# Kernel optimization log

Hardware: AMD Instinct MI355X
Metric: run time of the kernel (lower is better)

## Reference

```python
import jax, jax.numpy as jnp
import numpy as np

C = 512
GROUPS = 32
EPS = 1e-6


def setup_inputs() -> dict:
    key = jax.random.key(0)
    ks = jax.random.split(key, 10)
    B, H, W = 4, 64, 64
    s = 1.0 / np.sqrt(C)
    return {
        "x": jax.random.normal(ks[0], (B, C, H, W), dtype=jnp.float32),
        "gn_weight": jnp.ones((C,), jnp.float32),
        "gn_bias": jnp.zeros((C,), jnp.float32),
        "Wq": jax.random.normal(ks[1], (C, C), jnp.float32) * s,
        "bq": jnp.zeros((C,), jnp.float32),
        "Wk": jax.random.normal(ks[2], (C, C), jnp.float32) * s,
        "bk": jnp.zeros((C,), jnp.float32),
        "Wv": jax.random.normal(ks[3], (C, C), jnp.float32) * s,
        "bv": jnp.zeros((C,), jnp.float32),
        "Wo": jax.random.normal(ks[4], (C, C), jnp.float32) * s,
        "bo": jnp.zeros((C,), jnp.float32),
    }


def _group_norm(x, weight, bias):
    B, Ch, H, W = x.shape
    xg = x.reshape(B, GROUPS, Ch // GROUPS, H, W)
    mean = jnp.mean(xg, axis=(2, 3, 4), keepdims=True)
    var = jnp.var(xg, axis=(2, 3, 4), keepdims=True)
    xg = (xg - mean) * jax.lax.rsqrt(var + EPS)
    h = xg.reshape(B, Ch, H, W)
    return h * weight[None, :, None, None] + bias[None, :, None, None]


def reference(x, gn_weight, gn_bias, Wq, bq, Wk, bk, Wv, bv, Wo, bo):
    B, Ch, H, W = x.shape
    h = _group_norm(x, gn_weight, gn_bias)
    # [B, N, C] with N = H*W spatial tokens
    h = h.reshape(B, Ch, H * W).transpose(0, 2, 1)
    q = h @ Wq.T + bq
    k = h @ Wk.T + bk
    v = h @ Wv.T + bv
    scale = 1.0 / jnp.sqrt(jnp.asarray(Ch, x.dtype))
    scores = jnp.einsum("bnc,bmc->bnm", q, k) * scale  # [B, N, N]
    attn = jax.nn.softmax(scores, axis=-1)
    out = jnp.einsum("bnm,bmc->bnc", attn, v)
    out = out @ Wo.T + bo  # Dropout(0.0) is identity
    out = out.transpose(0, 2, 1).reshape(B, Ch, H, W)
    return x + out
```

## Files before the change

kernel.cpp:

```cpp
#include <hip/hip_runtime.h>
#include <hip/hip_bf16.h>

typedef __attribute__((ext_vector_type(8))) short bf16x8;
typedef __attribute__((ext_vector_type(4))) short bf16x4;
typedef __attribute__((ext_vector_type(4))) float f32x4;

__device__ __forceinline__ short f2bf(float f){
  __hip_bfloat16 h = __float2bfloat16(f);
  return __builtin_bit_cast(short, h);
}
__device__ __forceinline__ float bf2f(short s){
  unsigned u = ((unsigned)(unsigned short)s) << 16;
  return __builtin_bit_cast(float, u);
}

__device__ __forceinline__ void gload_lds16(const short* g, char* l){
  __builtin_amdgcn_global_load_lds(
      (const __attribute__((address_space(1))) void*)g,
      (__attribute__((address_space(3))) void*)l, 16, 0, 0);
}

#define SB0() __builtin_amdgcn_sched_barrier(0)
#define LGKM0() do{ asm volatile("s_waitcnt lgkmcnt(0)" ::: "memory"); SB0(); }while(0)
#define LGKM4() do{ asm volatile("s_waitcnt lgkmcnt(4)" ::: "memory"); SB0(); }while(0)

__global__ __launch_bounds__(256) void gn_stats(const float* __restrict__ x,
                                                float* __restrict__ stats){
  int b = blockIdx.x >> 5, g = blockIdx.x & 31;
  const float4* p = (const float4*)(x + ((long long)b*512 + g*16)*4096);
  float s = 0.f, s2 = 0.f;
  for (int i = threadIdx.x; i < 16384; i += 256){
    float4 v = p[i];
    s  += v.x + v.y + v.z + v.w;
    s2 += v.x*v.x + v.y*v.y + v.z*v.z + v.w*v.w;
  }
  #pragma unroll
  for (int o = 32; o; o >>= 1){ s += __shfl_xor(s, o); s2 += __shfl_xor(s2, o); }
  __shared__ float rs[4], rs2[4];
  int wid = threadIdx.x >> 6;
  if ((threadIdx.x & 63) == 0){ rs[wid] = s; rs2[wid] = s2; }
  __syncthreads();
  if (threadIdx.x == 0){
    float S  = rs[0]+rs[1]+rs[2]+rs[3];
    float S2 = rs2[0]+rs2[1]+rs2[2]+rs2[3];
    float mean = S * (1.f/65536.f);
    float var  = S2 * (1.f/65536.f) - mean*mean;
    stats[blockIdx.x*2]   = mean;
    stats[blockIdx.x*2+1] = rsqrtf(var + 1e-6f);
  }
}

__global__ __launch_bounds__(256) void gn_apply(const float* __restrict__ x,
                                                const float* __restrict__ stats,
                                                const float* __restrict__ gw,
                                                const float* __restrict__ gb,
                                                short* __restrict__ h){
  __shared__ float tile[128][65];
  int b  = blockIdx.y;
  int n0 = blockIdx.x * 64;
  int t  = threadIdx.x;
  const float* xb = x + (long long)b*512*4096;
  for (int cc = 0; cc < 4; cc++){
    int c0 = cc*128;
    #pragma unroll
    for (int r = 0; r < 128; r += 4){
      int c = r + (t >> 6);
      tile[c][t & 63] = xb[(long long)(c0+c)*4096 + n0 + (t & 63)];
    }
    __syncthreads();
    int n = t >> 2, cp = (t & 3)*32;
    short tmp[32];
    #pragma unroll
    for (int j = 0; j < 32; j++){
      int c = c0 + cp + j;
      float mean = stats[(b*32 + (c >> 4))*2];
      float rstd = stats[(b*32 + (c >> 4))*2 + 1];
      float v = (tile[cp+j][n] - mean)*rstd*gw[c] + gb[c];
      tmp[j] = f2bf(v);
    }
    long long ho = ((long long)b*4096 + n0 + n)*512 + c0 + cp;
    #pragma unroll
    for (int j2 = 0; j2 < 4; j2++){
      bf16x8 v8;
      #pragma unroll
      for (int e = 0; e < 8; e++) v8[e] = tmp[j2*8 + e];
      *(bf16x8*)&h[ho + j2*8] = v8;
    }
    __syncthreads();
  }
}

__global__ __launch_bounds__(256) void f2bf_all(
    const float* __restrict__ w0, const float* __restrict__ w1,
    const float* __restrict__ w2, const float* __restrict__ w3,
    short* __restrict__ o0, short* __restrict__ o1,
    short* __restrict__ o2, short* __restrict__ o3){
  int idx = blockIdx.x*256 + threadIdx.x;
  int m = idx >> 15, r = idx & 32767;
  const float* src = (m==0) ? w0 : (m==1) ? w1 : (m==2) ? w2 : w3;
  short* dst       = (m==0) ? o0 : (m==1) ? o1 : (m==2) ? o2 : o3;
  const float4* p = (const float4*)src + (long long)r*2;
  float4 a = p[0], c = p[1];
  bf16x8 v;
  v[0]=f2bf(a.x); v[1]=f2bf(a.y); v[2]=f2bf(a.z); v[3]=f2bf(a.w);
  v[4]=f2bf(c.x); v[5]=f2bf(c.y); v[6]=f2bf(c.z); v[7]=f2bf(c.w);
  *(bf16x8*)&dst[(long long)r*8] = v;
}

__global__ __launch_bounds__(256) void softmax_rows(short* __restrict__ S){
  long long row = blockIdx.x;
  short* p = S + row*4096;
  int t = threadIdx.x;
  bf16x8 v0 = *(bf16x8*)&p[t*16];
  bf16x8 v1 = *(bf16x8*)&p[t*16 + 8];
  float f[16];
  #pragma unroll
  for (int e = 0; e < 8; e++){ f[e] = bf2f(v0[e]); f[8+e] = bf2f(v1[e]); }
  float m = f[0];
  #pragma unroll
  for (int e = 1; e < 16; e++) m = fmaxf(m, f[e]);
  #pragma unroll
  for (int o = 32; o; o >>= 1) m = fmaxf(m, __shfl_xor(m, o));
  __shared__ float red[4];
  int wid = t >> 6;
  if ((t & 63) == 0) red[wid] = m;
  __syncthreads();
  m = fmaxf(fmaxf(red[0], red[1]), fmaxf(red[2], red[3]));
  float s = 0.f;
  #pragma unroll
  for (int e = 0; e < 16; e++){ f[e] = exp2f((f[e]-m)*1.4426950408889634f); s += f[e]; }
  #pragma unroll
  for (int o = 32; o; o >>= 1) s += __shfl_xor(s, o);
  __syncthreads();
  if ((t & 63) == 0) red[wid] = s;
  __syncthreads();
  s = red[0]+red[1]+red[2]+red[3];
  float inv = 1.f/s;
  #pragma unroll
  for (int e = 0; e < 8; e++){ v0[e] = f2bf(f[e]*inv); v1[e] = f2bf(f[8+e]*inv); }
  *(bf16x8*)&p[t*16]     = v0;
  *(bf16x8*)&p[t*16 + 8] = v1;
}

template<int MODE, int BN, bool SWZ>
__global__ __launch_bounds__(512, 2) void gemmP(
    const short* __restrict__ A, const short* __restrict__ Bw,
    const float* __restrict__ bias,
    void* __restrict__ outp, const float* __restrict__ resid,
    int M, int Nn, int Kd,
    long long sA, long long sB, long long sO, float scale)
{
  constexpr int WN = 64;
  constexpr int WARPS_N = BN/WN;
  constexpr int WARPS_M = 8/WARPS_N;
  constexpr int WM = 256/WARPS_M;
  constexpr int MF = WM/16;
  constexpr int MF2 = MF/2;
  constexpr int ABUF = 32768;
  constexpr int BBUF = BN*128;
  constexpr int BUFSZ = ABUF + BBUF;
  constexpr int BLOADS = BN/64;
  constexpr int LOADS = 4 + BLOADS;
  extern __shared__ char smem[];

  int bx, by, bz;
  if constexpr (SWZ){
    int id = blockIdx.x;
    int c = id & 7, s = id >> 3;
    int region = c + ((s >> 4) << 3);
    int o = s & 15;
    bz = region >> 4;
    bx = (region & 3)*4 + (o & 3);
    by = ((region >> 2) & 3)*4 + (o >> 2);
  } else { bx = blockIdx.x; by = blockIdx.y; bz = blockIdx.z; }

  const short* Ab = A + bz*sA;
  const short* Bb = Bw + bz*sB;
  const int m0 = bx*256, n0 = by*BN;
  const int t = threadIdx.x;
  const int lane = t & 63, wid = t >> 6;
  const int g = lane >> 4, lr = lane & 15;
  const int wr = wid / WARPS_N, wc = wid % WARPS_N;
  const long long KdLL = Kd;

  const int r0 = t >> 3;
  const int c0s = ((t & 7) ^ (r0 & 7)) * 8;
  const short* pA0 = Ab + (long long)(m0 + r0)*KdLL + c0s;
  const short* pB0 = Bb + (long long)(n0 + r0)*KdLL + c0s;

  int roA[MF], swA[MF], roB[4], swB[4];
  #pragma unroll
  for (int mf = 0; mf < MF; mf++){
    int ra = wr*WM + mf*16 + lr;
    roA[mf] = ra*128; swA[mf] = ra & 7;
  }
  #pragma unroll
  for (int nf = 0; nf < 4; nf++){
    int cb = wc*WN + nf*16 + lr;
    roB[nf] = ABUF + cb*128; swB[nf] = cb & 7;
  }

  f32x4 acc[MF][4];
  #pragma unroll
  for (int i = 0; i < MF; i++)
    #pragma unroll
    for (int j = 0; j < 4; j++)
      acc[i][j] = f32x4{0.f,0.f,0.f,0.f};
  bf16x8 av[MF2][2], bv[4][2];

  auto STAGE = [&](int kt, int buf){
    char* d = smem + buf*BUFSZ;
    const short* sa = pA0 + (long long)kt*64;
    #pragma unroll
    for (int j = 0; j < 4; j++)
      gload_lds16(sa + (long long)j*64*KdLL, d + j*8192 + t*16);
    const short* sb = pB0 + (long long)kt*64;
    #pragma unroll
    for (int j = 0; j < BLOADS; j++)
      gload_lds16(sb + (long long)j*64*KdLL, d + ABUF + j*8192 + t*16);
  };

  #define RD_AV(HI)                                                          \
    _Pragma("unroll")                                                        \
    for (int i = 0; i < MF2; i++){                                           \
      _Pragma("unroll")                                                      \
      for (int ks = 0; ks < 2; ks++)                                         \
        av[i][ks] = *(const bf16x8*)(base + roA[(HI)*MF2+i] +                \
                      ((((ks<<2)+g) ^ swA[(HI)*MF2+i])<<4));                 \
    }
  #define RD_BV(J0)                                                          \
    _Pragma("unroll")                                                        \
    for (int j = 0; j < 2; j++){                                             \
      _Pragma("unroll")                                                      \
      for (int ks = 0; ks < 2; ks++)                                         \
        bv[(J0)+j][ks] = *(const bf16x8*)(base + roB[(J0)+j] +               \
                      ((((ks<<2)+g) ^ swB[(J0)+j])<<4));                     \
    }
  #define QUAD(QM, QN)                                                       \
    __builtin_amdgcn_s_setprio(1);                                           \
    _Pragma("unroll")                                                        \
    for (int i = 0; i < MF2; i++)                                            \
      _Pragma("unroll")                                                      \
      for (int j = 0; j < 2; j++)                                            \
        _Pragma("unroll")                                                    \
        for (int ks = 0; ks < 2; ks++){                                      \
          if constexpr (MODE == 0)                                           \
            acc[(QM)*MF2+i][(QN)*2+j] = __builtin_amdgcn_mfma_f32_16x16x32_bf16( \
              bv[(QN)*2+j][ks], av[i][ks], acc[(QM)*MF2+i][(QN)*2+j], 0,0,0);\
          else                                                               \
            acc[(QM)*MF2+i][(QN)*2+j] = __builtin_amdgcn_mfma_f32_16x16x32_bf16( \
              av[i][ks], bv[(QN)*2+j][ks], acc[(QM)*MF2+i][(QN)*2+j], 0,0,0);\
        }                                                                    \
    __builtin_amdgcn_s_setprio(0);

  const int NT = Kd >> 6;

  STAGE(0, 0);
  STAGE(1, 1);
  if constexpr (LOADS == 8) asm volatile("s_waitcnt vmcnt(8)" ::: "memory");
  else                      asm volatile("s_waitcnt vmcnt(6)" ::: "memory");
  SB0();
  __builtin_amdgcn_s_barrier();

  for (int it = 0; it < NT; ++it){
    char* base = smem + (it & 1)*BUFSZ;
    const bool more = (it + 2 < NT);
    RD_AV(0); RD_BV(0); SB0();
    RD_BV(2); SB0();
    LGKM4();
    QUAD(0,0);
    LGKM0();
    QUAD(0,1);
    SB0();
    RD_AV(1); SB0();
    LGKM0();
    QUAD(1,0);
    SB0();
    __builtin_amdgcn_s_barrier();
    if (more) STAGE(it + 2, it & 1);
    QUAD(1,1);
    SB0();
    if (more){
      if constexpr (LOADS == 8) asm volatile("s_waitcnt vmcnt(8)" ::: "memory");
      else                      asm volatile("s_waitcnt vmcnt(6)" ::: "memory");
    } else {
      asm volatile("s_waitcnt vmcnt(0)" ::: "memory");
    }
    SB0();
    __builtin_amdgcn_s_barrier();
  }

  if constexpr (MODE == 0){
    short* outb = (short*)outp + bz*sO;
    const bool hb = (bias != nullptr);
    #pragma unroll
    for (int mi = 0; mi < MF; mi++){
      int row = m0 + wr*WM + mi*16 + lr;
      #pragma unroll
      for (int ni = 0; ni < 4; ni++){
        int col = n0 + wc*WN + ni*16 + g*4;
        float b0=0.f,b1=0.f,b2=0.f,b3=0.f;
        if (hb){ float4 bb = *(const float4*)&bias[col]; b0=bb.x; b1=bb.y; b2=bb.z; b3=bb.w; }
        bf16x4 pk;
        pk[0] = f2bf((acc[mi][ni][0] + b0)*scale);
        pk[1] = f2bf((acc[mi][ni][1] + b1)*scale);
        pk[2] = f2bf((acc[mi][ni][2] + b2)*scale);
        pk[3] = f2bf((acc[mi][ni][3] + b3)*scale);
        *(bf16x4*)&outb[(long long)row*Nn + col] = pk;
      }
    }
  } else if constexpr (MODE == 1){
    short* outb = (short*)outp + bz*sO;
    #pragma unroll
    for (int ni = 0; ni < 4; ni++){
      int col = n0 + wc*WN + ni*16 + lr;
      float bv2 = bias ? bias[col] : 0.f;
      #pragma unroll
      for (int mi = 0; mi < MF; mi++){
        int row = m0 + wr*WM + mi*16 + g*4;
        bf16x4 pk;
        #pragma unroll
        for (int i = 0; i < 4; i++) pk[i] = f2bf((acc[mi][ni][i] + bv2)*scale);
        *(bf16x4*)&outb[(long long)col*M + row] = pk;
      }
    }
  } else {
    float* outb = (float*)outp + bz*sO;
    const float* rx = resid + bz*sO;
    #pragma unroll
    for (int ni = 0; ni < 4; ni++){
      int col = n0 + wc*WN + ni*16 + lr;
      float bv2 = bias[col];
      #pragma unroll
      for (int mi = 0; mi < MF; mi++){
        int row = m0 + wr*WM + mi*16 + g*4;
        long long off = (long long)col*M + row;
        float4 xr = *(const float4*)&rx[off];
        float4 o;
        o.x = acc[mi][ni][0] + bv2 + xr.x;
        o.y = acc[mi][ni][1] + bv2 + xr.y;
        o.z = acc[mi][ni][2] + bv2 + xr.z;
        o.w = acc[mi][ni][3] + bv2 + xr.w;
        *(float4*)&outb[off] = o;
      }
    }
  }
  #undef RD_AV
  #undef RD_BV
  #undef QUAD
}

extern "C" void kernel_launch(void* const* d_in, const int* in_sizes, int n_in,
                              void* d_out, int out_size, void* d_ws, size_t ws_size,
                              hipStream_t stream)
{
  const float* x   = (const float*)d_in[0];
  const float* gnw = (const float*)d_in[1];
  const float* gnb = (const float*)d_in[2];
  const float* Wq  = (const float*)d_in[3];
  const float* bq  = (const float*)d_in[4];
  const float* Wk  = (const float*)d_in[5];
  const float* bk  = (const float*)d_in[6];
  const float* Wv  = (const float*)d_in[7];
  const float* bvp = (const float*)d_in[8];
  const float* Wo  = (const float*)d_in[9];
  const float* bo  = (const float*)d_in[10];
  float* out = (float*)d_out;

  char* ws = (char*)d_ws;
  const size_t MB = 1ull << 20;
  short* h    = (short*)(ws);
  short* q    = (short*)(ws + 16*MB);
  short* kmat = (short*)(ws + 32*MB);
  short* vt   = (short*)(ws + 48*MB);
  short* ao   = (short*)(ws + 64*MB);
  short* wqb  = (short*)(ws + 80*MB);
  short* wkb  = wqb + 262144;
  short* wvb  = wkb + 262144;
  short* wob  = wvb + 262144;
  float* stats= (float*)(ws + 82*MB);
  short* S    = (short*)(ws + 84*MB);

  const int LDS256 = 131072, LDS128 = 98304;
  hipFuncSetAttribute(reinterpret_cast<const void*>(&gemmP<0,256,true>),
                      hipFuncAttributeMaxDynamicSharedMemorySize, LDS256);
  hipFuncSetAttribute(reinterpret_cast<const void*>(&gemmP<0,128,false>),
                      hipFuncAttributeMaxDynamicSharedMemorySize, LDS128);
  hipFuncSetAttribute(reinterpret_cast<const void*>(&gemmP<1,128,false>),
                      hipFuncAttributeMaxDynamicSharedMemorySize, LDS128);
  hipFuncSetAttribute(reinterpret_cast<const void*>(&gemmP<2,128,false>),
                      hipFuncAttributeMaxDynamicSharedMemorySize, LDS128);

  dim3 blk(256);
  dim3 blk512(512);
  gn_stats<<<dim3(128), blk, 0, stream>>>(x, stats);
  gn_apply<<<dim3(64,4), blk, 0, stream>>>(x, stats, gnw, gnb, h);
  f2bf_all<<<dim3(512), blk, 0, stream>>>(Wq, Wk, Wv, Wo, wqb, wkb, wvb, wob);

  const long long sTok = 4096ll*512;
  const long long sS   = 4096ll*4096;
  const float qscale = 0.044194173824159216f;

  gemmP<0,128,false><<<dim3(16,4,4), blk512, LDS128, stream>>>(h, wqb, bq,  q,    nullptr, 4096, 512, 512, sTok, 0, sTok, qscale);
  gemmP<0,128,false><<<dim3(16,4,4), blk512, LDS128, stream>>>(h, wkb, bk,  kmat, nullptr, 4096, 512, 512, sTok, 0, sTok, 1.f);
  gemmP<1,128,false><<<dim3(16,4,4), blk512, LDS128, stream>>>(h, wvb, bvp, vt,   nullptr, 4096, 512, 512, sTok, 0, sTok, 1.f);

  if (ws_size >= 212*MB){
    gemmP<0,256,true><<<dim3(1024), blk512, LDS256, stream>>>(q, kmat, nullptr, S, nullptr, 4096, 4096, 512, sTok, sTok, sS, 1.f);
    softmax_rows<<<dim3(16384), blk, 0, stream>>>(S);
    gemmP<0,128,false><<<dim3(16,4,4), blk512, LDS128, stream>>>(S, vt, nullptr, ao, nullptr, 4096, 512, 4096, sS, sTok, sTok, 1.f);
  } else {
    for (int b = 0; b < 4; b++){
      gemmP<0,256,true><<<dim3(256), blk512, LDS256, stream>>>(q + b*sTok, kmat + b*sTok, nullptr, S, nullptr, 4096, 4096, 512, 0, 0, 0, 1.f);
      softmax_rows<<<dim3(4096), blk, 0, stream>>>(S);
      gemmP<0,128,false><<<dim3(16,4,1), blk512, LDS128, stream>>>(S, vt + b*sTok, nullptr, ao + b*sTok, nullptr, 4096, 512, 4096, 0, 0, 0, 1.f);
    }
  }

  gemmP<2,128,false><<<dim3(16,4,4), blk512, LDS128, stream>>>(ao, wob, bo, out, x, 4096, 512, 512, sTok, 0, sTok, 1.f);
}
```

Baseline: 344.3 us.

## Restructure GEMM main loop into four-phase pipelined schedule with split staging

The GEMM kernel's K-loop is rewritten into four MFMA phases per K tile. Each phase interleaves LDS fragment reads for the next quarter with half-tile global-to-LDS loads of the next A tile and the tile-after-next B tile, separated by workgroup barriers. The LDS layout is split into 128-row halves, and the swizzled block-to-XCD mapping for the QK^T GEMM is changed so each XCD owns a contiguous range of row tiles. The aim is to hide LDS and global latency behind MFMA work more finely, at the cost of many more barriers per iteration.

```diff
diff --git a/kernel.cpp b/kernel.cpp
--- a/kernel.cpp
+++ b/kernel.cpp
@@ -21,8 +21,7 @@
 }
 
 #define SB0() __builtin_amdgcn_sched_barrier(0)
-#define LGKM0() do{ asm volatile("s_waitcnt lgkmcnt(0)" ::: "memory"); SB0(); }while(0)
-#define LGKM4() do{ asm volatile("s_waitcnt lgkmcnt(4)" ::: "memory"); SB0(); }while(0)
+#define BARRIER() do{ SB0(); __builtin_amdgcn_s_barrier(); }while(0)
 
 __global__ __launch_bounds__(256) void gn_stats(const float* __restrict__ x,
                                                 float* __restrict__ stats){
@@ -143,35 +142,30 @@
 }
 
 template<int MODE, int BN, bool SWZ>
-__global__ __launch_bounds__(512, 2) void gemmP(
+__global__ __launch_bounds__(512, 2) void gemmF(
     const short* __restrict__ A, const short* __restrict__ Bw,
     const float* __restrict__ bias,
     void* __restrict__ outp, const float* __restrict__ resid,
     int M, int Nn, int Kd,
     long long sA, long long sB, long long sO, float scale)
 {
-  constexpr int WN = 64;
-  constexpr int WARPS_N = BN/WN;
+  constexpr int WARPS_N = BN/64;
   constexpr int WARPS_M = 8/WARPS_N;
   constexpr int WM = 256/WARPS_M;
   constexpr int MF = WM/16;
-  constexpr int MF2 = MF/2;
-  constexpr int ABUF = 32768;
-  constexpr int BBUF = BN*128;
-  constexpr int BUFSZ = ABUF + BBUF;
-  constexpr int BLOADS = BN/64;
-  constexpr int LOADS = 4 + BLOADS;
+  constexpr int QR = MF/4;
+  constexpr int ABYT = 32768;
+  constexpr int BBYT = BN*128;
+  constexpr int BUFSZ = ABYT + BBYT;
+  constexpr int BH = BBYT/16384;
   extern __shared__ char smem[];
 
   int bx, by, bz;
   if constexpr (SWZ){
     int id = blockIdx.x;
-    int c = id & 7, s = id >> 3;
-    int region = c + ((s >> 4) << 3);
-    int o = s & 15;
-    bz = region >> 4;
-    bx = (region & 3)*4 + (o & 3);
-    by = ((region >> 2) & 3)*4 + (o >> 2);
+    int xcd = id & 7, s = id >> 3;
+    int bxh = s >> 6, rem = s & 63;
+    bx = xcd*2 + bxh; by = rem & 15; bz = rem >> 4;
   } else { bx = blockIdx.x; by = blockIdx.y; bz = blockIdx.z; }
 
   const short* Ab = A + bz*sA;
@@ -183,21 +177,37 @@
   const int wr = wid / WARPS_N, wc = wid % WARPS_N;
   const long long KdLL = Kd;
 
-  const int r0 = t >> 3;
-  const int c0s = ((t & 7) ^ (r0 & 7)) * 8;
-  const short* pA0 = Ab + (long long)(m0 + r0)*KdLL + c0s;
-  const short* pB0 = Bb + (long long)(n0 + r0)*KdLL + c0s;
+  const int r0 = t >> 3, c8 = t & 7;
+
+  auto STAGE_A = [&](int kt, int buf, int h){
+    char* d = smem + buf*BUFSZ + h*16384 + t*16;
+    #pragma unroll
+    for (int j = 0; j < 2; j++){
+      int row = h*128 + j*64 + r0;
+      gload_lds16(Ab + (long long)(m0+row)*KdLL + (long long)kt*64 + ((c8 ^ (row&7))*8),
+                  d + j*8192);
+    }
+  };
+  auto STAGE_B = [&](int kt, int buf, int h){
+    char* d = smem + buf*BUFSZ + ABYT + h*16384 + t*16;
+    #pragma unroll
+    for (int j = 0; j < 2; j++){
+      int row = h*128 + j*64 + r0;
+      gload_lds16(Bb + (long long)(n0+row)*KdLL + (long long)kt*64 + ((c8 ^ (row&7))*8),
+                  d + j*8192);
+    }
+  };
 
   int roA[MF], swA[MF], roB[4], swB[4];
   #pragma unroll
   for (int mf = 0; mf < MF; mf++){
     int ra = wr*WM + mf*16 + lr;
-    roA[mf] = ra*128; swA[mf] = ra & 7;
+    roA[mf] = (ra>>7)*16384 + (ra&127)*128; swA[mf] = ra & 7;
   }
   #pragma unroll
   for (int nf = 0; nf < 4; nf++){
-    int cb = wc*WN + nf*16 + lr;
-    roB[nf] = ABUF + cb*128; swB[nf] = cb & 7;
+    int rb = wc*64 + nf*16 + lr;
+    roB[nf] = ABYT + (rb>>7)*16384 + (rb&127)*128; swB[nf] = rb & 7;
   }
 
   f32x4 acc[MF][4];
@@ -206,88 +216,92 @@
     #pragma unroll
     for (int j = 0; j < 4; j++)
       acc[i][j] = f32x4{0.f,0.f,0.f,0.f};
-  bf16x8 av[MF2][2], bv[4][2];
-
-  auto STAGE = [&](int kt, int buf){
-    char* d = smem + buf*BUFSZ;
-    const short* sa = pA0 + (long long)kt*64;
-    #pragma unroll
-    for (int j = 0; j < 4; j++)
-      gload_lds16(sa + (long long)j*64*KdLL, d + j*8192 + t*16);
-    const short* sb = pB0 + (long long)kt*64;
-    #pragma unroll
-    for (int j = 0; j < BLOADS; j++)
-      gload_lds16(sb + (long long)j*64*KdLL, d + ABUF + j*8192 + t*16);
-  };
-
-  #define RD_AV(HI)                                                          \
-    _Pragma("unroll")                                                        \
-    for (int i = 0; i < MF2; i++){                                           \
-      _Pragma("unroll")                                                      \
-      for (int ks = 0; ks < 2; ks++)                                         \
-        av[i][ks] = *(const bf16x8*)(base + roA[(HI)*MF2+i] +                \
-                      ((((ks<<2)+g) ^ swA[(HI)*MF2+i])<<4));                 \
-    }
-  #define RD_BV(J0)                                                          \
-    _Pragma("unroll")                                                        \
-    for (int j = 0; j < 2; j++){                                             \
-      _Pragma("unroll")                                                      \
-      for (int ks = 0; ks < 2; ks++)                                         \
-        bv[(J0)+j][ks] = *(const bf16x8*)(base + roB[(J0)+j] +               \
-                      ((((ks<<2)+g) ^ swB[(J0)+j])<<4));                     \
-    }
-  #define QUAD(QM, QN)                                                       \
-    __builtin_amdgcn_s_setprio(1);                                           \
-    _Pragma("unroll")                                                        \
-    for (int i = 0; i < MF2; i++)                                            \
-      _Pragma("unroll")                                                      \
-      for (int j = 0; j < 2; j++)                                            \
-        _Pragma("unroll")                                                    \
-        for (int ks = 0; ks < 2; ks++){                                      \
-          if constexpr (MODE == 0)                                           \
-            acc[(QM)*MF2+i][(QN)*2+j] = __builtin_amdgcn_mfma_f32_16x16x32_bf16( \
-              bv[(QN)*2+j][ks], av[i][ks], acc[(QM)*MF2+i][(QN)*2+j], 0,0,0);\
-          else                                                               \
-            acc[(QM)*MF2+i][(QN)*2+j] = __builtin_amdgcn_mfma_f32_16x16x32_bf16( \
-              av[i][ks], bv[(QN)*2+j][ks], acc[(QM)*MF2+i][(QN)*2+j], 0,0,0);\
-        }                                                                    \
-    __builtin_amdgcn_s_setprio(0);
+  bf16x8 av[2][QR][2], bv[4][2];
+
+  #define RD_AV(SET, Q, BASE) do{                                         \
+    _Pragma("unroll")                                                     \
+    for (int _i = 0; _i < QR; _i++)                                       \
+      _Pragma("unroll")                                                   \
+      for (int _ks = 0; _ks < 2; _ks++){                                  \
+        int _x = (Q)*QR + _i;                                             \
+        av[SET][_i][_ks] = *(const bf16x8*)((BASE) + roA[_x] +            \
+                            (((_ks*4+g) ^ swA[_x])<<4));                  \
+      } }while(0)
+
+  #define RD_BV(BASE) do{                                                 \
+    _Pragma("unroll")                                                     \
+    for (int _n = 0; _n < 4; _n++)                                        \
+      _Pragma("unroll")                                                   \
+      for (int _ks = 0; _ks < 2; _ks++)                                   \
+        bv[_n][_ks] = *(const bf16x8*)((BASE) + roB[_n] +                 \
+                            (((_ks*4+g) ^ swB[_n])<<4));                  \
+    }while(0)
+
+  #define MFMA_PH(Q, SET) do{                                             \
+    __builtin_amdgcn_s_setprio(1);                                        \
+    _Pragma("unroll")                                                     \
+    for (int _ks = 0; _ks < 2; _ks++)                                     \
+      _Pragma("unroll")                                                   \
+      for (int _n = 0; _n < 4; _n++)                                      \
+        _Pragma("unroll")                                                 \
+        for (int _i = 0; _i < QR; _i++){                                  \
+          if constexpr (MODE == 0)                                        \
+            acc[(Q)*QR+_i][_n] = __builtin_amdgcn_mfma_f32_16x16x32_bf16( \
+              bv[_n][_ks], av[SET][_i][_ks], acc[(Q)*QR+_i][_n], 0,0,0);  \
+          else                                                            \
+            acc[(Q)*QR+_i][_n] = __builtin_amdgcn_mfma_f32_16x16x32_bf16( \
+              av[SET][_i][_ks], bv[_n][_ks], acc[(Q)*QR+_i][_n], 0,0,0);  \
+        }                                                                 \
+    __builtin_amdgcn_s_setprio(0); }while(0)
+
+  #define WAIT_LGKM_JI() do{                                              \
+    if constexpr (QR == 2) asm volatile("s_waitcnt lgkmcnt(4)":::"memory");\
+    else                   asm volatile("s_waitcnt lgkmcnt(2)":::"memory");\
+    SB0(); }while(0)
 
   const int NT = Kd >> 6;
 
-  STAGE(0, 0);
-  STAGE(1, 1);
-  if constexpr (LOADS == 8) asm volatile("s_waitcnt vmcnt(8)" ::: "memory");
-  else                      asm volatile("s_waitcnt vmcnt(6)" ::: "memory");
+  STAGE_A(0,0,0); STAGE_A(0,0,1);
+  STAGE_B(0,0,0); if constexpr (BH==2) STAGE_B(0,0,1);
+  STAGE_B(1,1,0); if constexpr (BH==2) STAGE_B(1,1,1);
+  if constexpr (BH==2) asm volatile("s_waitcnt vmcnt(4)":::"memory");
+  else                 asm volatile("s_waitcnt vmcnt(2)":::"memory");
   SB0();
   __builtin_amdgcn_s_barrier();
-
-  for (int it = 0; it < NT; ++it){
-    char* base = smem + (it & 1)*BUFSZ;
-    const bool more = (it + 2 < NT);
-    RD_AV(0); RD_BV(0); SB0();
-    RD_BV(2); SB0();
-    LGKM4();
-    QUAD(0,0);
-    LGKM0();
-    QUAD(0,1);
+  RD_AV(0, 0, smem);
+
+  for (int kt = 0; kt < NT; ++kt){
+    char* bc  = smem + (kt & 1)*BUFSZ;
+    char* bn_ = smem + ((kt & 1)^1)*BUFSZ;
+    RD_BV(bc);
+    RD_AV(1, 1, bc);
+    if (kt+1 < NT) STAGE_A(kt+1, (kt&1)^1, 0);
+    BARRIER();
+    WAIT_LGKM_JI();
+    MFMA_PH(0, 0);
+    BARRIER();
+    RD_AV(0, 2, bc);
+    if (kt+1 < NT) STAGE_A(kt+1, (kt&1)^1, 1);
+    BARRIER();
+    WAIT_LGKM_JI();
+    MFMA_PH(1, 1);
+    BARRIER();
+    RD_AV(1, 3, bc);
+    if (kt+2 < NT) STAGE_B(kt+2, kt&1, 0);
+    BARRIER();
+    if (kt+2 < NT) asm volatile("s_waitcnt vmcnt(2)":::"memory");
+    else           asm volatile("s_waitcnt vmcnt(0)":::"memory");
     SB0();
-    RD_AV(1); SB0();
-    LGKM0();
-    QUAD(1,0);
-    SB0();
-    __builtin_amdgcn_s_barrier();
-    if (more) STAGE(it + 2, it & 1);
-    QUAD(1,1);
-    SB0();
-    if (more){
-      if constexpr (LOADS == 8) asm volatile("s_waitcnt vmcnt(8)" ::: "memory");
-      else                      asm volatile("s_waitcnt vmcnt(6)" ::: "memory");
-    } else {
-      asm volatile("s_waitcnt vmcnt(0)" ::: "memory");
-    }
-    SB0();
-    __builtin_amdgcn_s_barrier();
+    WAIT_LGKM_JI();
+    MFMA_PH(2, 0);
+    BARRIER();
+    if (kt+1 < NT) RD_AV(0, 0, bn_);
+    if constexpr (BH==2){ if (kt+2 < NT) STAGE_B(kt+2, kt&1, 1); }
+    BARRIER();
+    if (kt+1 < NT){ WAIT_LGKM_JI(); }
+    else { asm volatile("s_waitcnt lgkmcnt(0)":::"memory"); SB0(); }
+    MFMA_PH(3, 1);
+    BARRIER();
   }
 
   if constexpr (MODE == 0){
@@ -298,7 +312,7 @@
       int row = m0 + wr*WM + mi*16 + lr;
       #pragma unroll
       for (int ni = 0; ni < 4; ni++){
-        int col = n0 + wc*WN + ni*16 + g*4;
+        int col = n0 + wc*64 + ni*16 + g*4;
         float b0=0.f,b1=0.f,b2=0.f,b3=0.f;
         if (hb){ float4 bb = *(const float4*)&bias[col]; b0=bb.x; b1=bb.y; b2=bb.z; b3=bb.w; }
         bf16x4 pk;
@@ -313,7 +327,7 @@
     short* outb = (short*)outp + bz*sO;
     #pragma unroll
     for (int ni = 0; ni < 4; ni++){
-      int col = n0 + wc*WN + ni*16 + lr;
+      int col = n0 + wc*64 + ni*16 + lr;
       float bv2 = bias ? bias[col] : 0.f;
       #pragma unroll
       for (int mi = 0; mi < MF; mi++){
@@ -329,7 +343,7 @@
     const float* rx = resid + bz*sO;
     #pragma unroll
     for (int ni = 0; ni < 4; ni++){
-      int col = n0 + wc*WN + ni*16 + lr;
+      int col = n0 + wc*64 + ni*16 + lr;
       float bv2 = bias[col];
       #pragma unroll
       for (int mi = 0; mi < MF; mi++){
@@ -347,7 +361,8 @@
   }
   #undef RD_AV
   #undef RD_BV
-  #undef QUAD
+  #undef MFMA_PH
+  #undef WAIT_LGKM_JI
 }
 
 extern "C" void kernel_launch(void* const* d_in, const int* in_sizes, int n_in,
@@ -382,13 +397,15 @@
   short* S    = (short*)(ws + 84*MB);
 
   const int LDS256 = 131072, LDS128 = 98304;
-  hipFuncSetAttribute(reinterpret_cast<const void*>(&gemmP<0,256,true>),
+  hipFuncSetAttribute(reinterpret_cast<const void*>(&gemmF<0,256,true>),
                       hipFuncAttributeMaxDynamicSharedMemorySize, LDS256);
-  hipFuncSetAttribute(reinterpret_cast<const void*>(&gemmP<0,128,false>),
+  hipFuncSetAttribute(reinterpret_cast<const void*>(&gemmF<0,256,false>),
+                      hipFuncAttributeMaxDynamicSharedMemorySize, LDS256);
+  hipFuncSetAttribute(reinterpret_cast<const void*>(&gemmF<0,128,false>),
                       hipFuncAttributeMaxDynamicSharedMemorySize, LDS128);
-  hipFuncSetAttribute(reinterpret_cast<const void*>(&gemmP<1,128,false>),
+  hipFuncSetAttribute(reinterpret_cast<const void*>(&gemmF<1,128,false>),
                       hipFuncAttributeMaxDynamicSharedMemorySize, LDS128);
-  hipFuncSetAttribute(reinterpret_cast<const void*>(&gemmP<2,128,false>),
+  hipFuncSetAttribute(reinterpret_cast<const void*>(&gemmF<2,128,false>),
                       hipFuncAttributeMaxDynamicSharedMemorySize, LDS128);
 
   dim3 blk(256);
@@ -401,21 +418,21 @@
   const long long sS   = 4096ll*4096;
   const float qscale = 0.044194173824159216f;
 
-  gemmP<0,128,false><<<dim3(16,4,4), blk512, LDS128, stream>>>(h, wqb, bq,  q,    nullptr, 4096, 512, 512, sTok, 0, sTok, qscale);
-  gemmP<0,128,false><<<dim3(16,4,4), blk512, LDS128, stream>>>(h, wkb, bk,  kmat, nullptr, 4096, 512, 512, sTok, 0, sTok, 1.f);
-  gemmP<1,128,false><<<dim3(16,4,4), blk512, LDS128, stream>>>(h, wvb, bvp, vt,   nullptr, 4096, 512, 512, sTok, 0, sTok, 1.f);
+  gemmF<0,128,false><<<dim3(16,4,4), blk512, LDS128, stream>>>(h, wqb, bq,  q,    nullptr, 4096, 512, 512, sTok, 0, sTok, qscale);
+  gemmF<0,128,false><<<dim3(16,4,4), blk512, LDS128, stream>>>(h, wkb, bk,  kmat, nullptr, 4096, 512, 512, sTok, 0, sTok, 1.f);
+  gemmF<1,128,false><<<dim3(16,4,4), blk512, LDS128, stream>>>(h, wvb, bvp, vt,   nullptr, 4096, 512, 512, sTok, 0, sTok, 1.f);
 
   if (ws_size >= 212*MB){
-    gemmP<0,256,true><<<dim3(1024), blk512, LDS256, stream>>>(q, kmat, nullptr, S, nullptr, 4096, 4096, 512, sTok, sTok, sS, 1.f);
+    gemmF<0,256,true><<<dim3(1024), blk512, LDS256, stream>>>(q, kmat, nullptr, S, nullptr, 4096, 4096, 512, sTok, sTok, sS, 1.f);
     softmax_rows<<<dim3(16384), blk, 0, stream>>>(S);
-    gemmP<0,128,false><<<dim3(16,4,4), blk512, LDS128, stream>>>(S, vt, nullptr, ao, nullptr, 4096, 512, 4096, sS, sTok, sTok, 1.f);
+    gemmF<0,128,false><<<dim3(16,4,4), blk512, LDS128, stream>>>(S, vt, nullptr, ao, nullptr, 4096, 512, 4096, sS, sTok, sTok, 1.f);
   } else {
     for (int b = 0; b < 4; b++){
-      gemmP<0,256,true><<<dim3(256), blk512, LDS256, stream>>>(q + b*sTok, kmat + b*sTok, nullptr, S, nullptr, 4096, 4096, 512, 0, 0, 0, 1.f);
+      gemmF<0,256,false><<<dim3(16,16,1), blk512, LDS256, stream>>>(q + b*sTok, kmat + b*sTok, nullptr, S, nullptr, 4096, 4096, 512, 0, 0, 0, 1.f);
       softmax_rows<<<dim3(4096), blk, 0, stream>>>(S);
-      gemmP<0,128,false><<<dim3(16,4,1), blk512, LDS128, stream>>>(S, vt + b*sTok, nullptr, ao + b*sTok, nullptr, 4096, 512, 4096, 0, 0, 0, 1.f);
-    }
-  }
-
-  gemmP<2,128,false><<<dim3(16,4,4), blk512, LDS128, stream>>>(ao, wob, bo, out, x, 4096, 512, 512, sTok, 0, sTok, 1.f);
-}
+      gemmF<0,128,false><<<dim3(16,4,1), blk512, LDS128, stream>>>(S, vt + b*sTok, nullptr, ao + b*sTok, nullptr, 4096, 512, 4096, 0, 0, 0, 1.f);
+    }
+  }
+
+  gemmF<2,128,false><<<dim3(16,4,4), blk512, LDS128, stream>>>(ao, wob, bo, out, x, 4096, 512, 512, sTok, 0, sTok, 1.f);
+}
```

After: 360.7 us. 4.8% more time.
